# Kernel tuning notes

Measured on AMD Instinct MI355X. Metric: run time of the kernel, lower is better.

Reference implementation:

```python
import jax, jax.numpy as jnp
import numpy as np

N, E, D, HID, HEADS, G = 20000, 320000, 1280, 64, 4, 256
NEG_SLOPE = 0.2  # PyG GATv2Conv default negative_slope


def setup_inputs() -> dict:
    key = jax.random.key(0)
    ks = jax.random.split(key, 20)

    def w(k, shape, fan_in):
        return (jax.random.normal(k, shape, jnp.float32) / np.float32(np.sqrt(fan_in)))

    return {
        "x": jax.random.normal(ks[0], (N, D), jnp.float32),
        "edge_index": jax.random.randint(ks[1], (2, E), 0, N),
        "batch": jnp.sort(jax.random.randint(ks[2], (N,), 0, G)),
        # GATv2 layer 1: in D, out HID, heads HEADS, concat
        "Wl1": w(ks[3], (D, HEADS * HID), D),
        "bl1": w(ks[4], (HEADS * HID,), D),
        "Wr1": w(ks[5], (D, HEADS * HID), D),
        "br1": w(ks[6], (HEADS * HID,), D),
        "att1": w(ks[7], (HEADS, HID), HID),
        "bias1": jnp.zeros((HEADS * HID,), jnp.float32),
        # GATv2 layer 2: in HEADS*HID, out HID, heads 1, concat
        "Wl2": w(ks[8], (HEADS * HID, HID), HEADS * HID),
        "bl2": w(ks[9], (HID,), HEADS * HID),
        "Wr2": w(ks[10], (HEADS * HID, HID), HEADS * HID),
        "br2": w(ks[11], (HID,), HEADS * HID),
        "att2": w(ks[12], (1, HID), HID),
        "bias2": jnp.zeros((HID,), jnp.float32),
        # MLP head
        "W3": w(ks[13], (HID, HID), HID),
        "b3": w(ks[14], (HID,), HID),
        "W4": w(ks[15], (HID, 1), HID),
        "b4": w(ks[16], (1,), HID),
    }


def _gatv2(x, src, dst, Wl, bl, Wr, br, att, bias, n):
    """PyG GATv2Conv (concat=True, eval mode): e_ij = a^T LeakyReLU(Wl x_j + Wr x_i),
    per-destination softmax, out_i = sum_j alpha_ij * (Wl x_j)."""
    H, C = att.shape
    xl = (x @ Wl + bl).reshape(n, H, C)  # source transform
    xr = (x @ Wr + br).reshape(n, H, C)  # target transform
    e = jax.nn.leaky_relu(xl[src] + xr[dst], NEG_SLOPE)      # [E,H,C]
    logit = jnp.einsum('ehc,hc->eh', e, att)                  # [E,H]
    m = jax.ops.segment_max(logit, dst, num_segments=n)      # stable softmax per dst
    ex = jnp.exp(logit - m[dst])
    denom = jax.ops.segment_sum(ex, dst, num_segments=n)
    alpha = ex / (denom[dst] + 1e-16)                         # [E,H]
    out = jax.ops.segment_sum(xl[src] * alpha[:, :, None], dst, num_segments=n)
    return out.reshape(n, H * C) + bias


def reference(x, edge_index, batch, Wl1, bl1, Wr1, br1, att1, bias1,
              Wl2, bl2, Wr2, br2, att2, bias2, W3, b3, W4, b4):
    # add_self_loops=True (PyG default)
    loops = jnp.arange(N, dtype=edge_index.dtype)
    src = jnp.concatenate([edge_index[0], loops])
    dst = jnp.concatenate([edge_index[1], loops])
    h = jax.nn.relu(_gatv2(x, src, dst, Wl1, bl1, Wr1, br1, att1, bias1, N))
    h = jax.nn.relu(_gatv2(h, src, dst, Wl2, bl2, Wr2, br2, att2, bias2, N))
    g = jax.ops.segment_sum(h, batch, num_segments=G)  # global_add_pool -> [G,HID]
    return jax.nn.relu(g @ W3 + b3) @ W4 + b4          # [G,1]
```

## Files before the change

### kernel.cpp

```cpp
#include <hip/hip_runtime.h>

constexpr int Nn    = 20000;
constexpr int Ee    = 320000;
constexpr int Dd    = 1280;
constexpr int Gg    = 256;
constexpr int ETOT  = Ee + Nn;
#define NEG 0.2f

typedef __attribute__((ext_vector_type(8))) short s8v;
typedef __attribute__((ext_vector_type(8))) unsigned short u16x8;
typedef __attribute__((ext_vector_type(4))) float f4v;

__device__ inline float lrelu(float v){ return v > 0.f ? v : NEG * v; }
__device__ inline float wave_sum(float v){
  #pragma unroll
  for(int o = 32; o; o >>= 1) v += __shfl_xor(v, o, 64);
  return v;
}
__device__ inline unsigned short f2bf(float x){
  unsigned u = __float_as_uint(x);
  return (unsigned short)((u + 0x7FFFu + ((u >> 16) & 1u)) >> 16);
}
__device__ inline float bf2f(unsigned short h){ return __uint_as_float(((unsigned)h) << 16); }

__device__ inline void async_cp16(const void* g, void* l){
  __builtin_amdgcn_global_load_lds((const __attribute__((address_space(1))) void*)g,
                                   (__attribute__((address_space(3))) void*)l, 16, 0, 0);
}

__device__ inline size_t pkoff(int n, int k, int NITp){
  return ((((size_t)(n >> 7) * NITp + (k >> 5)) * 8 + ((n >> 4) & 7)) * 512)
       + (((n & 15) * 4 + ((k >> 3) & 3)) * 8) + (k & 7);
}

__global__ void fill_int(int* p, int n, int v){
  int i = blockIdx.x * blockDim.x + threadIdx.x;
  if(i < n) p[i] = v;
}
__global__ void hist_dst(const int* __restrict__ dst, int* __restrict__ deg){
  int e = blockIdx.x * blockDim.x + threadIdx.x;
  if(e < Ee) atomicAdd(&deg[dst[e]], 1);
}
__global__ __launch_bounds__(1024) void scan_deg(const int* __restrict__ deg,
                                                 int* __restrict__ rowptr,
                                                 int* __restrict__ cursor){
  __shared__ int part[1024];
  int t = threadIdx.x;
  const int CH = (Nn + 1023) / 1024;
  int base = t * CH;
  int s = 0;
  for(int j = 0; j < CH; j++){ int idx = base + j; if(idx < Nn) s += deg[idx]; }
  part[t] = s;
  __syncthreads();
  for(int off = 1; off < 1024; off <<= 1){
    int v = (t >= off) ? part[t - off] : 0;
    __syncthreads();
    part[t] += v;
    __syncthreads();
  }
  int acc = part[t] - s;
  for(int j = 0; j < CH; j++){
    int idx = base + j;
    if(idx < Nn){ rowptr[idx] = acc; cursor[idx] = acc; acc += deg[idx]; }
  }
  if(t == 1023) rowptr[Nn] = part[1023];
}
__global__ void scatter_edges(const int* __restrict__ src, const int* __restrict__ dst,
                              int* __restrict__ cursor, int* __restrict__ srcv){
  int e = blockIdx.x * blockDim.x + threadIdx.x;
  if(e >= ETOT) return;
  int d, s;
  if(e < Ee){ d = dst[e]; s = src[e]; } else { d = e - Ee; s = d; }
  int pos = atomicAdd(&cursor[d], 1);
  srcv[pos] = s;
}

__global__ __launch_bounds__(256) void wsplit(const float* __restrict__ Wl,
                                              const float* __restrict__ Wr,
                                              int K, int Ca, int NITp,
                                              unsigned short* __restrict__ PBH,
                                              unsigned short* __restrict__ PBL){
  __shared__ float t[32][33];
  int k0 = blockIdx.x * 32, n0 = blockIdx.y * 32;
  int tx = threadIdx.x & 31, ty = threadIdx.x >> 5;
  #pragma unroll
  for(int j = 0; j < 4; j++){
    int kk = ty + j * 8;
    int n = n0 + tx;
    t[kk][tx] = (n < Ca) ? Wl[(size_t)(k0 + kk) * Ca + n]
                         : Wr[(size_t)(k0 + kk) * Ca + (n - Ca)];
  }
  __syncthreads();
  #pragma unroll
  for(int j = 0; j < 4; j++){
    int nn = ty + j * 8;
    float v = t[tx][nn];
    unsigned short hi = f2bf(v);
    unsigned short lo = f2bf(v - bf2f(hi));
    size_t o = pkoff(n0 + nn, k0 + tx, NITp);
    PBH[o] = hi;
    PBL[o] = lo;
  }
}

__global__ __launch_bounds__(512) void gemm_2t(
    const float* __restrict__ X, int K, int niter,
    const unsigned short* __restrict__ PBH, const unsigned short* __restrict__ PBL,
    const float* __restrict__ bl, const float* __restrict__ br, int Ca,
    float* __restrict__ Ya, float* __restrict__ Yb)
{
  __shared__ unsigned short sA [2][128 * 32];
  __shared__ unsigned short sBh[2][128 * 32];
  __shared__ unsigned short sBl[2][128 * 32];

  const int tid  = threadIdx.x;
  const int lane = tid & 63;
  const int w    = tid >> 6;
  const int wm   = w & 1, wn = w >> 1;
  const int bm   = blockIdx.y * 128;
  const int bn   = blockIdx.x * 128;

  f4v acc[4][2] = {};

  const int ar = w * 16 + (lane >> 2);
  int gmr = bm + ar; if(gmr >= Nn) gmr = Nn - 1;
  const float* aptr = X + (size_t)gmr * K + (lane & 3) * 8;
  const int awoff = ar * 32 + (lane & 3) * 8;

  const size_t bbase = (((size_t)blockIdx.x * niter) * 8 + w) * 512 + lane * 8;
  const unsigned short* bhp = PBH + bbase;
  const unsigned short* blp = PBL + bbase;
  const int bldsoff = w * 512;

  async_cp16(bhp, &sBh[0][bldsoff]);
  async_cp16(blp, &sBl[0][bldsoff]);
  {
    float4 v0 = *(const float4*)(aptr);
    float4 v1 = *(const float4*)(aptr + 4);
    float fv[8] = {v0.x, v0.y, v0.z, v0.w, v1.x, v1.y, v1.z, v1.w};
    u16x8 hv;
    #pragma unroll
    for(int q = 0; q < 8; q++) hv[q] = f2bf(fv[q]);
    *(u16x8*)&sA[0][awoff] = hv;
  }

  const int mr = lane & 15;
  const int gq = lane >> 4;

  for(int it = 0; it < niter; it++){
    const int cur = it & 1, nxt = cur ^ 1;
    __syncthreads();
    float4 v0, v1;
    const bool more = (it + 1 < niter);
    if(more){
      async_cp16(bhp + (size_t)(it + 1) * 4096, &sBh[nxt][bldsoff]);
      async_cp16(blp + (size_t)(it + 1) * 4096, &sBl[nxt][bldsoff]);
      v0 = *(const float4*)(aptr + (it + 1) * 32);
      v1 = *(const float4*)(aptr + (it + 1) * 32 + 4);
    }
    s8v ah[4];
    #pragma unroll
    for(int i = 0; i < 4; i++)
      ah[i] = *(const s8v*)&sA[cur][(wm * 64 + i * 16 + mr) * 32 + gq * 8];
    #pragma unroll
    for(int j = 0; j < 2; j++){
      const int n = wn * 32 + j * 16 + mr;
      s8v bh  = *(const s8v*)&sBh[cur][n * 32 + gq * 8];
      s8v bl2 = *(const s8v*)&sBl[cur][n * 32 + gq * 8];
      #pragma unroll
      for(int i = 0; i < 4; i++){
        acc[i][j] = __builtin_amdgcn_mfma_f32_16x16x32_bf16(ah[i], bh,  acc[i][j], 0, 0, 0);
        acc[i][j] = __builtin_amdgcn_mfma_f32_16x16x32_bf16(ah[i], bl2, acc[i][j], 0, 0, 0);
      }
    }
    if(more){
      float fv[8] = {v0.x, v0.y, v0.z, v0.w, v1.x, v1.y, v1.z, v1.w};
      u16x8 hv;
      #pragma unroll
      for(int q = 0; q < 8; q++) hv[q] = f2bf(fv[q]);
      *(u16x8*)&sA[nxt][awoff] = hv;
    }
  }

  const int quad = lane >> 4, col = lane & 15;
  #pragma unroll
  for(int j = 0; j < 2; j++){
    int gn = bn + wn * 32 + j * 16 + col;
    const float* bias = (gn < Ca) ? bl : br;
    float*       Y    = (gn < Ca) ? Ya : Yb;
    int cn = gn & (Ca - 1);
    float bv = bias[cn];
    #pragma unroll
    for(int i = 0; i < 4; i++){
      #pragma unroll
      for(int rg = 0; rg < 4; rg++){
        int gmm = bm + wm * 64 + i * 16 + quad * 4 + rg;
        if(gmm < Nn) Y[(size_t)gmm * Ca + cn] = acc[i][j][rg] + bv;
      }
    }
  }
}

__global__ __launch_bounds__(256) void gat_fused1(
    const int* __restrict__ rowptr, const int* __restrict__ srcv,
    const float* __restrict__ XL, const float* __restrict__ XR,
    const float* __restrict__ att, const float* __restrict__ bias,
    float* __restrict__ H)
{
  int node = blockIdx.x * 4 + (threadIdx.x >> 6);
  int lane = threadIdx.x & 63;
  if(node >= Nn) return;
  const float4 xr = *(const float4*)(XR + (size_t)node * 256 + lane * 4);
  const float4 a  = *(const float4*)(att + lane * 4);
  int r0 = rowptr[node], r1 = rowptr[node + 1];
  float m[4], l[4]; float4 acc[4];
  #pragma unroll
  for(int c = 0; c < 4; c++){ m[c] = -1e30f; l[c] = 0.f; acc[c] = make_float4(0,0,0,0); }
  for(int k = r0; k < r1; k += 4){
    int nv = r1 - k;
    int s[4]; float4 xl[4]; float p[4];
    #pragma unroll
    for(int c = 0; c < 4; c++){
      int kk = (c < nv) ? (k + c) : k;
      s[c] = srcv[kk];
    }
    #pragma unroll
    for(int c = 0; c < 4; c++) xl[c] = *(const float4*)(XL + (size_t)s[c] * 256 + lane * 4);
    #pragma unroll
    for(int c = 0; c < 4; c++){
      p[c] = lrelu(xl[c].x + xr.x) * a.x + lrelu(xl[c].y + xr.y) * a.y
           + lrelu(xl[c].z + xr.z) * a.z + lrelu(xl[c].w + xr.w) * a.w;
    }
    #pragma unroll
    for(int o = 8; o; o >>= 1){
      #pragma unroll
      for(int c = 0; c < 4; c++) p[c] += __shfl_xor(p[c], o, 64);
    }
    #pragma unroll
    for(int c = 0; c < 4; c++){
      if(c < nv){
        float mn = fmaxf(m[c], p[c]);
        float sc = __expf(m[c] - mn);
        float wg = __expf(p[c] - mn);
        l[c] = l[c] * sc + wg;
        acc[c].x = acc[c].x * sc + wg * xl[c].x;
        acc[c].y = acc[c].y * sc + wg * xl[c].y;
        acc[c].z = acc[c].z * sc + wg * xl[c].z;
        acc[c].w = acc[c].w * sc + wg * xl[c].w;
        m[c] = mn;
      }
    }
  }
  float M = fmaxf(fmaxf(m[0], m[1]), fmaxf(m[2], m[3]));
  float L = 0.f; float4 A4 = make_float4(0,0,0,0);
  #pragma unroll
  for(int c = 0; c < 4; c++){
    float sc = __expf(m[c] - M);
    L += l[c] * sc;
    A4.x += acc[c].x * sc; A4.y += acc[c].y * sc;
    A4.z += acc[c].z * sc; A4.w += acc[c].w * sc;
  }
  float inv = 1.f / (L + 1e-16f);
  const float4 b = *(const float4*)(bias + lane * 4);
  float4 o;
  o.x = fmaxf(A4.x * inv + b.x, 0.f);
  o.y = fmaxf(A4.y * inv + b.y, 0.f);
  o.z = fmaxf(A4.z * inv + b.z, 0.f);
  o.w = fmaxf(A4.w * inv + b.w, 0.f);
  *(float4*)(H + (size_t)node * 256 + lane * 4) = o;
}

__global__ __launch_bounds__(256) void gat_fused2(
    const int* __restrict__ rowptr, const int* __restrict__ srcv,
    const float* __restrict__ XL, const float* __restrict__ XR,
    const float* __restrict__ att, const float* __restrict__ bias,
    float* __restrict__ H)
{
  int node = blockIdx.x * 4 + (threadIdx.x >> 6);
  int lane = threadIdx.x & 63;
  if(node >= Nn) return;
  const float xr = XR[(size_t)node * 64 + lane];
  const float a = att[lane];
  int r0 = rowptr[node], r1 = rowptr[node + 1];
  float m[4], l[4], acc[4];
  #pragma unroll
  for(int c = 0; c < 4; c++){ m[c] = -1e30f; l[c] = 0.f; acc[c] = 0.f; }
  for(int k = r0; k < r1; k += 4){
    int nv = r1 - k;
    int s[4]; float xl[4]; float p[4];
    #pragma unroll
    for(int c = 0; c < 4; c++){
      int kk = (c < nv) ? (k + c) : k;
      s[c] = srcv[kk];
    }
    #pragma unroll
    for(int c = 0; c < 4; c++) xl[c] = XL[(size_t)s[c] * 64 + lane];
    #pragma unroll
    for(int c = 0; c < 4; c++) p[c] = lrelu(xl[c] + xr) * a;
    #pragma unroll
    for(int o = 32; o; o >>= 1){
      #pragma unroll
      for(int c = 0; c < 4; c++) p[c] += __shfl_xor(p[c], o, 64);
    }
    #pragma unroll
    for(int c = 0; c < 4; c++){
      if(c < nv){
        float mn = fmaxf(m[c], p[c]);
        float sc = __expf(m[c] - mn);
        float wg = __expf(p[c] - mn);
        l[c] = l[c] * sc + wg;
        acc[c] = acc[c] * sc + wg * xl[c];
        m[c] = mn;
      }
    }
  }
  float M = fmaxf(fmaxf(m[0], m[1]), fmaxf(m[2], m[3]));
  float L = 0.f, A1 = 0.f;
  #pragma unroll
  for(int c = 0; c < 4; c++){
    float sc = __expf(m[c] - M);
    L += l[c] * sc; A1 += acc[c] * sc;
  }
  float inv = 1.f / (L + 1e-16f);
  H[(size_t)node * 64 + lane] = fmaxf(A1 * inv + bias[lane], 0.f);
}

__global__ void gbounds(const int* __restrict__ batch, int* __restrict__ gs){
  int g = blockIdx.x * blockDim.x + threadIdx.x;
  if(g > Gg) return;
  int lo = 0, hi = Nn;
  while(lo < hi){ int mid = (lo + hi) >> 1; if(batch[mid] < g) lo = mid + 1; else hi = mid; }
  gs[g] = lo;
}
__global__ __launch_bounds__(64) void pool_seg(const float* __restrict__ H2,
                                               const int* __restrict__ gs,
                                               float* __restrict__ GP){
  int g = blockIdx.x, t = threadIdx.x;
  int i0 = gs[g], i1 = gs[g + 1];
  float a0 = 0.f, a1 = 0.f, a2 = 0.f, a3 = 0.f;
  int i = i0;
  for(; i + 3 < i1; i += 4){
    a0 += H2[(size_t)i * 64 + t];       a1 += H2[(size_t)(i + 1) * 64 + t];
    a2 += H2[(size_t)(i + 2) * 64 + t]; a3 += H2[(size_t)(i + 3) * 64 + t];
  }
  for(; i < i1; i++) a0 += H2[(size_t)i * 64 + t];
  GP[(size_t)g * 64 + t] = (a0 + a1) + (a2 + a3);
}
__global__ __launch_bounds__(64) void mlp_head(const float* __restrict__ GP,
                                               const float* __restrict__ W3,
                                               const float* __restrict__ b3,
                                               const float* __restrict__ W4,
                                               const float* __restrict__ b4,
                                               float* __restrict__ out){
  int g = blockIdx.x;
  int j = threadIdx.x;
  __shared__ float sh[64];
  sh[j] = GP[(size_t)g * 64 + j];
  __syncthreads();
  float t = b3[j];
  #pragma unroll
  for(int k = 0; k < 64; k++) t = fmaf(sh[k], W3[k * 64 + j], t);
  t = fmaxf(t, 0.f);
  float p = t * W4[j];
  p = wave_sum(p);
  if(j == 0) out[g] = p + b4[0];
}

extern "C" void kernel_launch(void* const* d_in, const int* in_sizes, int n_in,
                              void* d_out, int out_size, void* d_ws, size_t ws_size,
                              hipStream_t stream)
{
  const float* x     = (const float*)d_in[0];
  const int*   ei    = (const int*)d_in[1];
  const int*   batch = (const int*)d_in[2];
  const float* Wl1   = (const float*)d_in[3];
  const float* bl1   = (const float*)d_in[4];
  const float* Wr1   = (const float*)d_in[5];
  const float* br1   = (const float*)d_in[6];
  const float* att1  = (const float*)d_in[7];
  const float* bias1 = (const float*)d_in[8];
  const float* Wl2   = (const float*)d_in[9];
  const float* bl2   = (const float*)d_in[10];
  const float* Wr2   = (const float*)d_in[11];
  const float* br2   = (const float*)d_in[12];
  const float* att2  = (const float*)d_in[13];
  const float* bias2 = (const float*)d_in[14];
  const float* W3    = (const float*)d_in[15];
  const float* b3    = (const float*)d_in[16];
  const float* W4    = (const float*)d_in[17];
  const float* b4    = (const float*)d_in[18];
  float* out = (float*)d_out;

  char* ws = (char*)d_ws;
  size_t off = 0;
  auto alloc = [&](size_t bytes) -> void* {
    void* p = ws + off;
    off += (bytes + 255) & ~(size_t)255;
    return p;
  };
  float* XL1  = (float*)alloc((size_t)Nn * 256 * 4);
  float* XR1  = (float*)alloc((size_t)Nn * 256 * 4);
  float* H1   = (float*)alloc((size_t)Nn * 256 * 4);
  unsigned short* PB1H = (unsigned short*)alloc((size_t)512 * Dd * 2);
  unsigned short* PB1L = (unsigned short*)alloc((size_t)512 * Dd * 2);
  unsigned short* PB2H = (unsigned short*)alloc((size_t)128 * 256 * 2);
  unsigned short* PB2L = (unsigned short*)alloc((size_t)128 * 256 * 2);
  int*   rowptr = (int*)alloc((size_t)(Nn + 1) * 4);
  int*   deg    = (int*)alloc((size_t)Nn * 4);
  int*   cursor = (int*)alloc((size_t)Nn * 4);
  int*   srcv   = (int*)alloc((size_t)ETOT * 4);
  float* H2   = (float*)alloc((size_t)Nn * 64 * 4);
  float* GP   = (float*)alloc((size_t)Gg * 64 * 4);
  int*   gs   = (int*)alloc((size_t)(Gg + 1) * 4);
  float* XL2 = XL1;
  float* XR2 = XR1;

  const int* srcA = ei;
  const int* dstA = ei + Ee;

  fill_int<<<(Nn + 255) / 256, 256, 0, stream>>>(deg, Nn, 1);
  hist_dst<<<(Ee + 255) / 256, 256, 0, stream>>>(dstA, deg);
  scan_deg<<<1, 1024, 0, stream>>>(deg, rowptr, cursor);
  scatter_edges<<<(ETOT + 255) / 256, 256, 0, stream>>>(srcA, dstA, cursor, srcv);
  gbounds<<<1, 512, 0, stream>>>(batch, gs);

  wsplit<<<dim3(Dd / 32, 512 / 32), 256, 0, stream>>>(Wl1, Wr1, Dd, 256, Dd / 32, PB1H, PB1L);
  wsplit<<<dim3(256 / 32, 128 / 32), 256, 0, stream>>>(Wl2, Wr2, 256, 64, 256 / 32, PB2H, PB2L);

  gemm_2t<<<dim3(4, (Nn + 127) / 128), 512, 0, stream>>>(
      x, Dd, Dd / 32, PB1H, PB1L, bl1, br1, 256, XL1, XR1);
  gat_fused1<<<(Nn + 3) / 4, 256, 0, stream>>>(rowptr, srcv, XL1, XR1, att1, bias1, H1);

  gemm_2t<<<dim3(1, (Nn + 127) / 128), 512, 0, stream>>>(
      H1, 256, 256 / 32, PB2H, PB2L, bl2, br2, 64, XL2, XR2);
  gat_fused2<<<(Nn + 3) / 4, 256, 0, stream>>>(rowptr, srcv, XL2, XR2, att2, bias2, H2);

  pool_seg<<<Gg, 64, 0, stream>>>(H2, gs, GP);
  mlp_head<<<Gg, 64, 0, stream>>>(GP, W3, b3, W4, b4, out);
}
```

Baseline: 473.8 us.

## Swizzle GEMM LDS layout, repack weights k-major, and remap blocks for L2 reuse

Repacks the split bf16 weight tiles k-group-major so each thread loads a contiguous 16-byte chunk. Stores the A tile in LDS with a k-group-major, row-rotated layout to reduce bank conflicts on the MFMA fragment reads. LDS offsets are precomputed once outside the loop. The layer-1 GEMM moves to a 1D grid that groups 8 row tiles with all 4 column tiles, so neighbouring blocks share X rows in cache; a bounds check covers the padded blocks.

Result: no change. 466.1 us (-1.6%).

```diff
diff --git a/kernel.cpp b/kernel.cpp
--- a/kernel.cpp
+++ b/kernel.cpp
@@ -29,8 +29,8 @@
 }
 
 __device__ inline size_t pkoff(int n, int k, int NITp){
-  return ((((size_t)(n >> 7) * NITp + (k >> 5)) * 8 + ((n >> 4) & 7)) * 512)
-       + (((n & 15) * 4 + ((k >> 3) & 3)) * 8) + (k & 7);
+  return ((((size_t)(n >> 7) * NITp + (k >> 5)) * 512)
+          + (((k >> 3) & 3) * 128 + (n & 127))) * 8 + (k & 7);
 }
 
 __global__ void fill_int(int* p, int n, int v){
@@ -104,30 +104,39 @@
 }
 
 __global__ __launch_bounds__(512) void gemm_2t(
-    const float* __restrict__ X, int K, int niter,
+    const float* __restrict__ X, int K, int niter, int ntx, int nty,
     const unsigned short* __restrict__ PBH, const unsigned short* __restrict__ PBL,
     const float* __restrict__ bl, const float* __restrict__ br, int Ca,
     float* __restrict__ Ya, float* __restrict__ Yb)
 {
-  __shared__ unsigned short sA [2][128 * 32];
-  __shared__ unsigned short sBh[2][128 * 32];
-  __shared__ unsigned short sBl[2][128 * 32];
+  int xb, yb;
+  if(ntx == 4){
+    int id = blockIdx.x;
+    int g = id >> 5, rem = id & 31;
+    xb = rem >> 3; yb = g * 8 + (rem & 7);
+  } else { xb = 0; yb = blockIdx.x; }
+  if(yb >= nty) return;
+
+  __shared__ unsigned short sA [2][4096];
+  __shared__ unsigned short sBh[2][4096];
+  __shared__ unsigned short sBl[2][4096];
 
   const int tid  = threadIdx.x;
   const int lane = tid & 63;
   const int w    = tid >> 6;
   const int wm   = w & 1, wn = w >> 1;
-  const int bm   = blockIdx.y * 128;
-  const int bn   = blockIdx.x * 128;
+  const int bm   = yb * 128;
+  const int bn   = xb * 128;
 
   f4v acc[4][2] = {};
 
   const int ar = w * 16 + (lane >> 2);
+  const int aq = lane & 3;
   int gmr = bm + ar; if(gmr >= Nn) gmr = Nn - 1;
-  const float* aptr = X + (size_t)gmr * K + (lane & 3) * 8;
-  const int awoff = ar * 32 + (lane & 3) * 8;
-
-  const size_t bbase = (((size_t)blockIdx.x * niter) * 8 + w) * 512 + lane * 8;
+  const float* aptr = X + (size_t)gmr * K + aq * 8;
+  const int awoff = (aq * 128 + ((ar + aq * 4) & 127)) * 8;
+
+  const size_t bbase = ((size_t)xb * niter) * 4096 + tid * 8;
   const unsigned short* bhp = PBH + bbase;
   const unsigned short* blp = PBL + bbase;
   const int bldsoff = w * 512;
@@ -146,6 +155,17 @@
 
   const int mr = lane & 15;
   const int gq = lane >> 4;
+  int aoff[4], boff[2];
+  #pragma unroll
+  for(int i = 0; i < 4; i++){
+    int row = wm * 64 + i * 16 + mr;
+    aoff[i] = (gq * 128 + ((row + gq * 4) & 127)) * 8;
+  }
+  #pragma unroll
+  for(int j = 0; j < 2; j++){
+    int n = wn * 32 + j * 16 + mr;
+    boff[j] = (gq * 128 + n) * 8;
+  }
 
   for(int it = 0; it < niter; it++){
     const int cur = it & 1, nxt = cur ^ 1;
@@ -160,13 +180,11 @@
     }
     s8v ah[4];
     #pragma unroll
-    for(int i = 0; i < 4; i++)
-      ah[i] = *(const s8v*)&sA[cur][(wm * 64 + i * 16 + mr) * 32 + gq * 8];
+    for(int i = 0; i < 4; i++) ah[i] = *(const s8v*)&sA[cur][aoff[i]];
     #pragma unroll
     for(int j = 0; j < 2; j++){
-      const int n = wn * 32 + j * 16 + mr;
-      s8v bh  = *(const s8v*)&sBh[cur][n * 32 + gq * 8];
-      s8v bl2 = *(const s8v*)&sBl[cur][n * 32 + gq * 8];
+      s8v bh  = *(const s8v*)&sBh[cur][boff[j]];
+      s8v bl2 = *(const s8v*)&sBl[cur][boff[j]];
       #pragma unroll
       for(int i = 0; i < 4; i++){
         acc[i][j] = __builtin_amdgcn_mfma_f32_16x16x32_bf16(ah[i], bh,  acc[i][j], 0, 0, 0);
@@ -427,12 +445,12 @@
   wsplit<<<dim3(Dd / 32, 512 / 32), 256, 0, stream>>>(Wl1, Wr1, Dd, 256, Dd / 32, PB1H, PB1L);
   wsplit<<<dim3(256 / 32, 128 / 32), 256, 0, stream>>>(Wl2, Wr2, 256, 64, 256 / 32, PB2H, PB2L);
 
-  gemm_2t<<<dim3(4, (Nn + 127) / 128), 512, 0, stream>>>(
-      x, Dd, Dd / 32, PB1H, PB1L, bl1, br1, 256, XL1, XR1);
+  gemm_2t<<<640, 512, 0, stream>>>(
+      x, Dd, Dd / 32, 4, (Nn + 127) / 128, PB1H, PB1L, bl1, br1, 256, XL1, XR1);
   gat_fused1<<<(Nn + 3) / 4, 256, 0, stream>>>(rowptr, srcv, XL1, XR1, att1, bias1, H1);
 
-  gemm_2t<<<dim3(1, (Nn + 127) / 128), 512, 0, stream>>>(
-      H1, 256, 256 / 32, PB2H, PB2L, bl2, br2, 64, XL2, XR2);
+  gemm_2t<<<(Nn + 127) / 128, 512, 0, stream>>>(
+      H1, 256, 256 / 32, 1, (Nn + 127) / 128, PB2H, PB2L, bl2, br2, 64, XL2, XR2);
   gat_fused2<<<(Nn + 3) / 4, 256, 0, stream>>>(rowptr, srcv, XL2, XR2, att2, bias2, H2);
 
   pool_seg<<<Gg, 64, 0, stream>>>(H2, gs, GP);
```
